# Performance work log

Hardware: AMD Instinct MI355X
Metric: run time of the kernel (lower is better)

The kernel has to match this reference:

```python
import jax, jax.numpy as jnp
import numpy as np

N_NODES = 100000
N_EDGES = 1600000
IN_C, HID_C, OUT_C = 256, 128, 64


def sage_conv(x, src, dst, Wl, Wr, b, n_nodes):
    """PyG SAGEConv: lin_l(mean of neighbor messages) + lin_r(x) + b."""
    msgs = x[src]  # [E, C] gather
    agg = jax.ops.segment_sum(msgs, dst, num_segments=n_nodes)  # [N, C] scatter-add
    deg = jax.ops.segment_sum(jnp.ones((src.shape[0],), x.dtype), dst, num_segments=n_nodes)
    agg = agg / jnp.maximum(deg, 1.0)[:, None]  # mean aggregation, safe for isolated nodes
    return agg @ Wl + x @ Wr + b


def setup_inputs() -> dict:
    key = jax.random.key(0)
    ks = jax.random.split(key, 12)

    def glorot(k, shape):
        fan_in, fan_out = shape
        lim = float(np.sqrt(6.0 / (fan_in + fan_out)))
        return jax.random.uniform(k, shape, jnp.float32, -lim, lim)

    x = jax.random.normal(ks[0], (N_NODES, IN_C), jnp.float32)
    edge_index = jax.random.randint(ks[1], (2, N_EDGES), 0, N_NODES, jnp.int32)
    return {
        "x": x,
        "edge_index": edge_index,
        "Wl0": glorot(ks[2], (IN_C, HID_C)),
        "Wr0": glorot(ks[3], (IN_C, HID_C)),
        "b0": jnp.zeros((HID_C,), jnp.float32),
        "Wl1": glorot(ks[4], (HID_C, HID_C)),
        "Wr1": glorot(ks[5], (HID_C, HID_C)),
        "b1": jnp.zeros((HID_C,), jnp.float32),
        "Wl2": glorot(ks[6], (HID_C, OUT_C)),
        "Wr2": glorot(ks[7], (HID_C, OUT_C)),
        "b2": jnp.zeros((OUT_C,), jnp.float32),
    }


def reference(x, edge_index, Wl0, Wr0, b0, Wl1, Wr1, b1, Wl2, Wr2, b2):
    src, dst = edge_index[0], edge_index[1]
    n = x.shape[0]
    h = x
    out = None
    # convs[:-1]: conv -> relu -> dropout (eval mode: dropout = identity)
    for Wl, Wr, b in ((Wl0, Wr0, b0), (Wl1, Wr1, b1)):
        out = sage_conv(h, src, dst, Wl, Wr, b, n)
        h = jax.nn.relu(out)
    g = h
    x_final = sage_conv(g, src, dst, Wl2, Wr2, b2, n)
    return (x_final, out, g)
```

## Files before the change

### kernel.cpp

```cpp
#include <hip/hip_runtime.h>
#include <stdint.h>

typedef __attribute__((ext_vector_type(4))) float f32x4;
typedef _Float16 half8 __attribute__((ext_vector_type(8)));
typedef _Float16 half4 __attribute__((ext_vector_type(4)));


#define BIN_CHUNK 8192
#define MAXB 512

__global__ __launch_bounds__(256) void k_bhist(const int* __restrict__ dst,
                                               int* __restrict__ bcnt, int E) {
    __shared__ int lh[MAXB];
    for (int i = threadIdx.x; i < MAXB; i += 256) lh[i] = 0;
    __syncthreads();
    const int base = blockIdx.x * BIN_CHUNK;
#pragma unroll 4
    for (int i = 0; i < BIN_CHUNK / 256; i++) {
        int e = base + i * 256 + threadIdx.x;
        if (e < E) atomicAdd(&lh[dst[e] >> 8], 1);
    }
    __syncthreads();
    for (int i = threadIdx.x; i < MAXB; i += 256)
        if (lh[i]) atomicAdd(&bcnt[i], lh[i]);
}

__global__ void k_bscan(const int* __restrict__ bcnt, int* __restrict__ bbase,
                        int* __restrict__ gcur, int nb) {
    if (threadIdx.x == 0 && blockIdx.x == 0) {
        int run = 0;
        for (int i = 0; i < nb; i++) { bbase[i] = run; gcur[i] = run; run += bcnt[i]; }
        bbase[nb] = run;
    }
}

__global__ __launch_bounds__(256) void k_bin(const int* __restrict__ src,
                                             const int* __restrict__ dst,
                                             int* __restrict__ gcur,
                                             unsigned* __restrict__ ebuf, int E) {
    __shared__ int lh[MAXB];
    __shared__ int lcur[MAXB];
    for (int i = threadIdx.x; i < MAXB; i += 256) lh[i] = 0;
    __syncthreads();
    const int base = blockIdx.x * BIN_CHUNK;
#pragma unroll 4
    for (int i = 0; i < BIN_CHUNK / 256; i++) {
        int e = base + i * 256 + threadIdx.x;
        if (e < E) atomicAdd(&lh[dst[e] >> 8], 1);
    }
    __syncthreads();
    for (int i = threadIdx.x; i < MAXB; i += 256)
        lcur[i] = lh[i] ? atomicAdd(&gcur[i], lh[i]) : 0;
    __syncthreads();
#pragma unroll 4
    for (int i = 0; i < BIN_CHUNK / 256; i++) {
        int e = base + i * 256 + threadIdx.x;
        if (e < E) {
            int d = dst[e];
            int pos = atomicAdd(&lcur[d >> 8], 1);
            ebuf[pos] = (unsigned)src[e] | ((unsigned)(d & 255) << 24);
        }
    }
}

__global__ __launch_bounds__(256) void k_nhist(const unsigned* __restrict__ ebuf,
                                               const int* __restrict__ bbase,
                                               int* __restrict__ deg, int N) {
    __shared__ int cnt[256];
    cnt[threadIdx.x] = 0;
    __syncthreads();
    const int b = blockIdx.x;
    const int lo = bbase[b], hi = bbase[b + 1];
    for (int e = lo + threadIdx.x; e < hi; e += 256)
        atomicAdd(&cnt[ebuf[e] >> 24], 1);
    __syncthreads();
    int n = (b << 8) + threadIdx.x;
    if (n < N) deg[n] = cnt[threadIdx.x];
}

__global__ __launch_bounds__(256) void k_bfill(const unsigned* __restrict__ ebuf,
                                               const int* __restrict__ bbase,
                                               const int* __restrict__ rowptr,
                                               int* __restrict__ ssrc, int N) {
    __shared__ int lc[256];
    const int b = blockIdx.x;
    int n = (b << 8) + threadIdx.x;
    lc[threadIdx.x] = (n < N) ? rowptr[n] : 0;
    __syncthreads();
    const int lo = bbase[b], hi = bbase[b + 1];
    for (int e = lo + threadIdx.x; e < hi; e += 256) {
        unsigned v = ebuf[e];
        int pos = atomicAdd(&lc[v >> 24], 1);
        ssrc[pos] = (int)(v & 0xFFFFFFu);
    }
}


__global__ void k_scan1(int* __restrict__ buf, int* __restrict__ chunkSum, int N) {
    const int t = threadIdx.x;
    const int base = blockIdx.x * 2048 + t * 8;
    int v[8];
    int s = 0;
#pragma unroll
    for (int i = 0; i < 8; i++) {
        int idx = base + i;
        v[i] = (idx < N) ? buf[idx] : 0;
        s += v[i];
    }
    __shared__ int sh[256];
    sh[t] = s;
    __syncthreads();
    for (int off = 1; off < 256; off <<= 1) {
        int add = (t >= off) ? sh[t - off] : 0;
        __syncthreads();
        sh[t] += add;
        __syncthreads();
    }
    int excl = sh[t] - s;
    int run = excl;
#pragma unroll
    for (int i = 0; i < 8; i++) {
        int idx = base + i;
        if (idx < N) buf[idx] = run;
        run += v[i];
    }
    if (t == 255) chunkSum[blockIdx.x] = sh[255];
}

__global__ void k_scan2(const int* __restrict__ chunkSum, int* __restrict__ chunkOff,
                        int nch, int* __restrict__ rowptrN) {
    if (threadIdx.x == 0 && blockIdx.x == 0) {
        int run = 0;
        for (int i = 0; i < nch; i++) { chunkOff[i] = run; run += chunkSum[i]; }
        *rowptrN = run;
    }
}

__global__ void k_scan3(int* __restrict__ rowptr, const int* __restrict__ chunkOff, int N) {
    int i = blockIdx.x * 256 + threadIdx.x;
    if (i < N) rowptr[i] += chunkOff[i >> 11];
}


template <int K, int NCOLT>
__global__ void k_wprep(const float* __restrict__ Wl, const float* __restrict__ Wr,
                        _Float16* __restrict__ Wt) {
    constexpr int NCOL = NCOLT / 2;
    int i = blockIdx.x * 256 + threadIdx.x;
    if (i < K * NCOLT) {
        int n = i / K, k = i - n * K;
        float v = (n < NCOL) ? Wl[(size_t)k * NCOL + n] : Wr[(size_t)k * NCOL + (n - NCOL)];
        Wt[(size_t)(k >> 5) * (NCOLT * 32) + n * 32 + (k & 31)] = (_Float16)v;
    }
}


template <int K, int NCOLT, bool AF32>
__global__ __launch_bounds__(256) void k_gemmM(const void* __restrict__ Av,
                                               const _Float16* __restrict__ Wt,
                                               const float* __restrict__ bias,
                                               _Float16* __restrict__ Cl,
                                               _Float16* __restrict__ Cr, int M) {
    constexpr int NCOL = NCOLT / 2;
    constexpr int WC = NCOLT / 4;
    constexpr int NT = WC / 16;
    constexpr int AS = K + 8;
    constexpr int CS = NCOLT + 8;
    constexpr int MAXS = (K > NCOLT ? K : NCOLT) + 8;
    __shared__ _Float16 sh[64 * MAXS];

    const int tid = threadIdx.x;
    const int lane = tid & 63;
    const int wave = tid >> 6;
    const int quad = lane >> 4;
    const int l16 = lane & 15;
    const int m0 = blockIdx.x * 64;
    const int colbase = wave * WC;

    if (AF32) {
        const float* A = (const float*)Av;
#pragma unroll
        for (int i = 0; i < K / 16; i++) {
            int off = i * 1024 + tid * 4;
            int row = off / K, col = off % K;
            f32x4 u = {0.f, 0.f, 0.f, 0.f};
            if (m0 + row < M) u = *(const f32x4*)(A + (size_t)(m0 + row) * K + col);
            half4 h = {(_Float16)u[0], (_Float16)u[1], (_Float16)u[2], (_Float16)u[3]};
            *(half4*)(sh + row * AS + col) = h;
        }
    } else {
        const _Float16* A = (const _Float16*)Av;
#pragma unroll
        for (int i = 0; i < K / 32; i++) {
            int off = i * 2048 + tid * 8;
            int row = off / K, col = off % K;
            half8 u = {0, 0, 0, 0, 0, 0, 0, 0};
            if (m0 + row < M) u = *(const half8*)(A + (size_t)(m0 + row) * K + col);
            *(half8*)(sh + row * AS + col) = u;
        }
    }
    __syncthreads();

    f32x4 acc[4][NT];
#pragma unroll
    for (int rg = 0; rg < 4; rg++)
#pragma unroll
        for (int t = 0; t < NT; t++) acc[rg][t] = (f32x4){0.f, 0.f, 0.f, 0.f};

#pragma unroll
    for (int k0 = 0; k0 < K; k0 += 32) {
        half8 a[4];
#pragma unroll
        for (int rg = 0; rg < 4; rg++)
            a[rg] = *(const half8*)(sh + (rg * 16 + l16) * AS + k0 + quad * 8);
        half8 b[NT];
        const _Float16* Wk = Wt + (size_t)(k0 >> 5) * (NCOLT * 32);
#pragma unroll
        for (int t = 0; t < NT; t++)
            b[t] = *(const half8*)(Wk + (colbase + t * 16 + l16) * 32 + quad * 8);
#pragma unroll
        for (int rg = 0; rg < 4; rg++)
#pragma unroll
            for (int t = 0; t < NT; t++)
                acc[rg][t] = __builtin_amdgcn_mfma_f32_16x16x32_f16(b[t], a[rg], acc[rg][t], 0, 0, 0);
    }

    __syncthreads();

#pragma unroll
    for (int t = 0; t < NT; t++) {
        int c0 = colbase + t * 16 + quad * 4;
        f32x4 bv = {0.f, 0.f, 0.f, 0.f};
        if (c0 >= NCOL) bv = *(const f32x4*)(bias + (c0 - NCOL));
#pragma unroll
        for (int rg = 0; rg < 4; rg++) {
            half4 h = {(_Float16)(acc[rg][t][0] + bv[0]), (_Float16)(acc[rg][t][1] + bv[1]),
                       (_Float16)(acc[rg][t][2] + bv[2]), (_Float16)(acc[rg][t][3] + bv[3])};
            *(half4*)(sh + (rg * 16 + l16) * CS + c0) = h;
        }
    }
    __syncthreads();

#pragma unroll
    for (int i = 0; i < (64 * NCOL) / 2048; i++) {
        int off = i * 2048 + tid * 8;
        int row = off / NCOL, col = off % NCOL;
        if (m0 + row < M) {
            *(half8*)(Cl + (size_t)(m0 + row) * NCOL + col) = *(const half8*)(sh + row * CS + col);
            *(half8*)(Cr + (size_t)(m0 + row) * NCOL + col) = *(const half8*)(sh + row * CS + NCOL + col);
        }
    }
}


template <int COUT, int MODE>
__global__ __launch_bounds__(256) void k_agg(const half8* __restrict__ xl,
                                             const half8* __restrict__ xr,
                                             const int* __restrict__ rowptr,
                                             const int* __restrict__ ssrc,
                                             float* __restrict__ outF1,
                                             float* __restrict__ outF2,
                                             _Float16* __restrict__ outH, int N) {
    constexpr int LPN = COUT / 16;
    constexpr int NPB = 256 / LPN;
    constexpr int C8 = COUT / 8;
    const int tid = threadIdx.x;
    const int c = tid % LPN;
    const int n = blockIdx.x * NPB + tid / LPN;
    if (n >= N) return;

    const int rp0 = rowptr[n];
    const int rp1 = rowptr[n + 1];
    float acc[16];
#pragma unroll
    for (int i = 0; i < 16; i++) acc[i] = 0.f;

    const size_t cb = (size_t)c * 2;
    int e = rp0;
    for (; e + 3 < rp1; e += 4) {
        int s0 = ssrc[e], s1 = ssrc[e + 1], s2 = ssrc[e + 2], s3 = ssrc[e + 3];
        half8 v0a = xl[(size_t)s0 * C8 + cb], v0b = xl[(size_t)s0 * C8 + cb + 1];
        half8 v1a = xl[(size_t)s1 * C8 + cb], v1b = xl[(size_t)s1 * C8 + cb + 1];
        half8 v2a = xl[(size_t)s2 * C8 + cb], v2b = xl[(size_t)s2 * C8 + cb + 1];
        half8 v3a = xl[(size_t)s3 * C8 + cb], v3b = xl[(size_t)s3 * C8 + cb + 1];
#pragma unroll
        for (int i = 0; i < 8; i++) {
            acc[i] += (float)v0a[i] + (float)v1a[i] + (float)v2a[i] + (float)v3a[i];
            acc[8 + i] += (float)v0b[i] + (float)v1b[i] + (float)v2b[i] + (float)v3b[i];
        }
    }
    for (; e < rp1; e++) {
        int s = ssrc[e];
        half8 va = xl[(size_t)s * C8 + cb], vb = xl[(size_t)s * C8 + cb + 1];
#pragma unroll
        for (int i = 0; i < 8; i++) {
            acc[i] += (float)va[i];
            acc[8 + i] += (float)vb[i];
        }
    }

    const int deg = rp1 - rp0;
    const float scale = 1.0f / (float)(deg > 1 ? deg : 1);
    half8 x0 = xr[(size_t)n * C8 + cb];
    half8 x1 = xr[(size_t)n * C8 + cb + 1];
    float res[16];
#pragma unroll
    for (int i = 0; i < 8; i++) {
        res[i] = acc[i] * scale + (float)x0[i];
        res[8 + i] = acc[8 + i] * scale + (float)x1[i];
    }

    const size_t ob = (size_t)n * COUT + (size_t)c * 16;
    if (MODE == 0) {
        half8 h0v, h1v;
#pragma unroll
        for (int i = 0; i < 8; i++) {
            h0v[i] = (_Float16)(res[i] > 0.f ? res[i] : 0.f);
            h1v[i] = (_Float16)(res[8 + i] > 0.f ? res[8 + i] : 0.f);
        }
        *(half8*)(outH + ob) = h0v;
        *(half8*)(outH + ob + 8) = h1v;
    } else if (MODE == 1) {
#pragma unroll
        for (int q = 0; q < 4; q++) {
            f32x4 v = {res[q * 4], res[q * 4 + 1], res[q * 4 + 2], res[q * 4 + 3]};
            *(f32x4*)(outF1 + ob + q * 4) = v;
            f32x4 z = {v[0] > 0.f ? v[0] : 0.f, v[1] > 0.f ? v[1] : 0.f,
                       v[2] > 0.f ? v[2] : 0.f, v[3] > 0.f ? v[3] : 0.f};
            *(f32x4*)(outF2 + ob + q * 4) = z;
        }
        half8 h0v, h1v;
#pragma unroll
        for (int i = 0; i < 8; i++) {
            h0v[i] = (_Float16)(res[i] > 0.f ? res[i] : 0.f);
            h1v[i] = (_Float16)(res[8 + i] > 0.f ? res[8 + i] : 0.f);
        }
        *(half8*)(outH + ob) = h0v;
        *(half8*)(outH + ob + 8) = h1v;
    } else {
#pragma unroll
        for (int q = 0; q < 4; q++) {
            f32x4 v = {res[q * 4], res[q * 4 + 1], res[q * 4 + 2], res[q * 4 + 3]};
            *(f32x4*)(outF1 + ob + q * 4) = v;
        }
    }
}


extern "C" void kernel_launch(void* const* d_in, const int* in_sizes, int n_in,
                              void* d_out, int out_size, void* d_ws, size_t ws_size,
                              hipStream_t stream) {
    const float* x   = (const float*)d_in[0];
    const int*   ei  = (const int*)d_in[1];
    const float* Wl0 = (const float*)d_in[2];
    const float* Wr0 = (const float*)d_in[3];
    const float* b0  = (const float*)d_in[4];
    const float* Wl1 = (const float*)d_in[5];
    const float* Wr1 = (const float*)d_in[6];
    const float* b1  = (const float*)d_in[7];
    const float* Wl2 = (const float*)d_in[8];
    const float* Wr2 = (const float*)d_in[9];
    const float* b2  = (const float*)d_in[10];

    const int N = in_sizes[0] / 256;
    const int E = in_sizes[1] / 2;
    const int* src = ei;
    const int* dst = ei + E;

    char* p = (char*)d_ws;
    auto alloc = [&](size_t bytes) -> void* {
        void* r = (void*)p;
        p += (bytes + 255) & ~(size_t)255;
        return r;
    };
    int*      rowptr   = (int*)alloc((size_t)(N + 1) * 4);
    int*      chunkSum = (int*)alloc(64 * 4);
    int*      chunkOff = (int*)alloc(64 * 4);
    int*      bcnt     = (int*)alloc(MAXB * 4);
    int*      bbase    = (int*)alloc((MAXB + 1) * 4);
    int*      gcur     = (int*)alloc(MAXB * 4);
    int*      ssrc     = (int*)alloc((size_t)E * 4);
    _Float16* xl       = (_Float16*)alloc((size_t)N * 128 * 2);
    _Float16* xr       = (_Float16*)alloc((size_t)N * 128 * 2);
    _Float16* h0       = (_Float16*)alloc((size_t)N * 128 * 2);
    _Float16* gb       = (_Float16*)alloc((size_t)N * 128 * 2);
    _Float16* Wt0      = (_Float16*)alloc((size_t)256 * 256 * 2);
    _Float16* Wt1      = (_Float16*)alloc((size_t)256 * 128 * 2);
    _Float16* Wt2      = (_Float16*)alloc((size_t)128 * 128 * 2);

    unsigned* ebuf = (unsigned*)gb;

    float* out = (float*)d_out;
    float* x_final = out;
    float* out1    = out + (size_t)N * 64;
    float* g       = out + (size_t)N * 192;

    const int nb = (N + 255) >> 8;
    const int nbk = (E + BIN_CHUNK - 1) / BIN_CHUNK;

    hipMemsetAsync(bcnt, 0, MAXB * 4, stream);
    k_bhist<<<nbk, 256, 0, stream>>>(dst, bcnt, E);
    k_bscan<<<1, 64, 0, stream>>>(bcnt, bbase, gcur, nb);
    k_bin<<<nbk, 256, 0, stream>>>(src, dst, gcur, ebuf, E);
    k_nhist<<<nb, 256, 0, stream>>>(ebuf, bbase, rowptr, N);
    int nch = (N + 2047) / 2048;
    k_scan1<<<nch, 256, 0, stream>>>(rowptr, chunkSum, N);
    k_scan2<<<1, 64, 0, stream>>>(chunkSum, chunkOff, nch, rowptr + N);
    k_scan3<<<(N + 255) / 256, 256, 0, stream>>>(rowptr, chunkOff, N);
    k_bfill<<<nb, 256, 0, stream>>>(ebuf, bbase, rowptr, ssrc, N);

    k_wprep<256, 256><<<(256 * 256 + 255) / 256, 256, 0, stream>>>(Wl0, Wr0, Wt0);
    k_wprep<128, 256><<<(128 * 256 + 255) / 256, 256, 0, stream>>>(Wl1, Wr1, Wt1);
    k_wprep<128, 128><<<(128 * 128 + 255) / 256, 256, 0, stream>>>(Wl2, Wr2, Wt2);

    const int gGrid = (N + 63) / 64;

    k_gemmM<256, 256, true><<<gGrid, 256, 0, stream>>>(x, Wt0, b0, xl, xr, N);
    k_agg<128, 0><<<(N + 31) / 32, 256, 0, stream>>>((const half8*)xl, (const half8*)xr,
                                                     rowptr, ssrc, nullptr, nullptr, h0, N);

    k_gemmM<128, 256, false><<<gGrid, 256, 0, stream>>>(h0, Wt1, b1, xl, xr, N);
    k_agg<128, 1><<<(N + 31) / 32, 256, 0, stream>>>((const half8*)xl, (const half8*)xr,
                                                     rowptr, ssrc, out1, g, gb, N);

    k_gemmM<128, 128, false><<<gGrid, 256, 0, stream>>>(gb, Wt2, b2, xl, xr, N);
    k_agg<64, 2><<<(N + 63) / 64, 256, 0, stream>>>((const half8*)xl, (const half8*)xr,
                                                    rowptr, ssrc, x_final, nullptr, nullptr, N);
}
```

Before: 578.6 us.

## Balance edge work across threads in aggregation via shared-memory atomic accumulation

The aggregation kernel no longer gives each node group its own node's edges. It divides the block's contiguous edge range evenly among thread groups, finds each group's starting node by binary search over cached row pointers, and accumulates partial sums into a shared-memory float buffer with atomics. The goal is to remove warp divergence and load imbalance from uneven node degrees. In exchange it adds a block barrier, shared-memory atomics at segment boundaries, and extra LDS traffic.

```diff
diff --git a/kernel.cpp b/kernel.cpp
--- a/kernel.cpp
+++ b/kernel.cpp
@@ -254,63 +254,103 @@
 
 
 template <int COUT, int MODE>
-__global__ __launch_bounds__(256) void k_agg(const half8* __restrict__ xl,
-                                             const half8* __restrict__ xr,
+__global__ __launch_bounds__(256) void k_agg(const _Float16* __restrict__ xl,
+                                             const _Float16* __restrict__ xr,
                                              const int* __restrict__ rowptr,
                                              const int* __restrict__ ssrc,
                                              float* __restrict__ outF1,
                                              float* __restrict__ outF2,
                                              _Float16* __restrict__ outH, int N) {
     constexpr int LPN = COUT / 16;
-    constexpr int NPB = 256 / LPN;
-    constexpr int C8 = COUT / 8;
+    constexpr int NB = 256 / LPN;
+    constexpr int AP = COUT + 4;
+    __shared__ float acc[NB * AP];
+    __shared__ int rp[NB + 1];
+
     const int tid = threadIdx.x;
+    const int n0 = blockIdx.x * NB;
+    if (tid <= NB) {
+        int nn = n0 + tid;
+        rp[tid] = rowptr[nn < N ? nn : N];
+    }
+    for (int i = tid; i < NB * AP; i += 256) acc[i] = 0.f;
+    __syncthreads();
+
+    const int lo = rp[0];
+    const int B = rp[NB] - lo;
+    const int g = tid / LPN;
     const int c = tid % LPN;
-    const int n = blockIdx.x * NPB + tid / LPN;
+    const int cb = c * 16;
+
+    int e0 = lo + (int)(((long long)B * g) / NB);
+    int e1 = lo + (int)(((long long)B * (g + 1)) / NB);
+
+    if (e0 < e1) {
+        int jl = 0, jh = NB - 1;
+        while (jl < jh) {
+            int mid = (jl + jh) >> 1;
+            if (rp[mid + 1] <= e0) jl = mid + 1; else jh = mid;
+        }
+        int j = jl;
+        float racc[16];
+#pragma unroll
+        for (int i = 0; i < 16; i++) racc[i] = 0.f;
+
+        int e = e0;
+        while (e < e1) {
+            int ee = rp[j + 1];
+            if (ee > e1) ee = e1;
+            for (; e + 3 < ee; e += 4) {
+                int s0 = ssrc[e], s1 = ssrc[e + 1], s2 = ssrc[e + 2], s3 = ssrc[e + 3];
+                const half8* p0 = (const half8*)(xl + (size_t)s0 * COUT + cb);
+                const half8* p1 = (const half8*)(xl + (size_t)s1 * COUT + cb);
+                const half8* p2 = (const half8*)(xl + (size_t)s2 * COUT + cb);
+                const half8* p3 = (const half8*)(xl + (size_t)s3 * COUT + cb);
+                half8 v0a = p0[0], v0b = p0[1];
+                half8 v1a = p1[0], v1b = p1[1];
+                half8 v2a = p2[0], v2b = p2[1];
+                half8 v3a = p3[0], v3b = p3[1];
+#pragma unroll
+                for (int i = 0; i < 8; i++) {
+                    racc[i] += (float)v0a[i] + (float)v1a[i] + (float)v2a[i] + (float)v3a[i];
+                    racc[8 + i] += (float)v0b[i] + (float)v1b[i] + (float)v2b[i] + (float)v3b[i];
+                }
+            }
+            for (; e < ee; e++) {
+                int s = ssrc[e];
+                const half8* p = (const half8*)(xl + (size_t)s * COUT + cb);
+                half8 va = p[0], vb = p[1];
+#pragma unroll
+                for (int i = 0; i < 8; i++) {
+                    racc[i] += (float)va[i];
+                    racc[8 + i] += (float)vb[i];
+                }
+            }
+#pragma unroll
+            for (int i = 0; i < 16; i++) {
+                atomicAdd(&acc[j * AP + cb + i], racc[i]);
+                racc[i] = 0.f;
+            }
+            while (j < NB - 1 && rp[j + 1] <= e) j++;
+        }
+    }
+    __syncthreads();
+
+    const int node = tid / LPN;
+    const int n = n0 + node;
     if (n >= N) return;
-
-    const int rp0 = rowptr[n];
-    const int rp1 = rowptr[n + 1];
-    float acc[16];
-#pragma unroll
-    for (int i = 0; i < 16; i++) acc[i] = 0.f;
-
-    const size_t cb = (size_t)c * 2;
-    int e = rp0;
-    for (; e + 3 < rp1; e += 4) {
-        int s0 = ssrc[e], s1 = ssrc[e + 1], s2 = ssrc[e + 2], s3 = ssrc[e + 3];
-        half8 v0a = xl[(size_t)s0 * C8 + cb], v0b = xl[(size_t)s0 * C8 + cb + 1];
-        half8 v1a = xl[(size_t)s1 * C8 + cb], v1b = xl[(size_t)s1 * C8 + cb + 1];
-        half8 v2a = xl[(size_t)s2 * C8 + cb], v2b = xl[(size_t)s2 * C8 + cb + 1];
-        half8 v3a = xl[(size_t)s3 * C8 + cb], v3b = xl[(size_t)s3 * C8 + cb + 1];
-#pragma unroll
-        for (int i = 0; i < 8; i++) {
-            acc[i] += (float)v0a[i] + (float)v1a[i] + (float)v2a[i] + (float)v3a[i];
-            acc[8 + i] += (float)v0b[i] + (float)v1b[i] + (float)v2b[i] + (float)v3b[i];
-        }
-    }
-    for (; e < rp1; e++) {
-        int s = ssrc[e];
-        half8 va = xl[(size_t)s * C8 + cb], vb = xl[(size_t)s * C8 + cb + 1];
-#pragma unroll
-        for (int i = 0; i < 8; i++) {
-            acc[i] += (float)va[i];
-            acc[8 + i] += (float)vb[i];
-        }
-    }
-
-    const int deg = rp1 - rp0;
+    const int deg = rp[node + 1] - rp[node];
     const float scale = 1.0f / (float)(deg > 1 ? deg : 1);
-    half8 x0 = xr[(size_t)n * C8 + cb];
-    half8 x1 = xr[(size_t)n * C8 + cb + 1];
+    const half8* xp = (const half8*)(xr + (size_t)n * COUT + cb);
+    half8 x0 = xp[0], x1 = xp[1];
     float res[16];
 #pragma unroll
     for (int i = 0; i < 8; i++) {
-        res[i] = acc[i] * scale + (float)x0[i];
-        res[8 + i] = acc[8 + i] * scale + (float)x1[i];
-    }
-
-    const size_t ob = (size_t)n * COUT + (size_t)c * 16;
+        res[i] = acc[node * AP + cb + i] * scale + (float)x0[i];
+        res[8 + i] = acc[node * AP + cb + 8 + i] * scale + (float)x1[i];
+    }
+
+    const size_t ob = (size_t)n * COUT + cb;
     if (MODE == 0) {
         half8 h0v, h1v;
 #pragma unroll
@@ -416,14 +456,14 @@
     const int gGrid = (N + 63) / 64;
 
     k_gemmM<256, 256, true><<<gGrid, 256, 0, stream>>>(x, Wt0, b0, xl, xr, N);
-    k_agg<128, 0><<<(N + 31) / 32, 256, 0, stream>>>((const half8*)xl, (const half8*)xr,
-                                                     rowptr, ssrc, nullptr, nullptr, h0, N);
+    k_agg<128, 0><<<(N + 31) / 32, 256, 0, stream>>>(xl, xr, rowptr, ssrc,
+                                                     nullptr, nullptr, h0, N);
 
     k_gemmM<128, 256, false><<<gGrid, 256, 0, stream>>>(h0, Wt1, b1, xl, xr, N);
-    k_agg<128, 1><<<(N + 31) / 32, 256, 0, stream>>>((const half8*)xl, (const half8*)xr,
-                                                     rowptr, ssrc, out1, g, gb, N);
+    k_agg<128, 1><<<(N + 31) / 32, 256, 0, stream>>>(xl, xr, rowptr, ssrc,
+                                                     out1, g, gb, N);
 
     k_gemmM<128, 128, false><<<gGrid, 256, 0, stream>>>(gb, Wt2, b2, xl, xr, N);
-    k_agg<64, 2><<<(N + 63) / 64, 256, 0, stream>>>((const half8*)xl, (const half8*)xr,
-                                                    rowptr, ssrc, x_final, nullptr, nullptr, N);
-}
+    k_agg<64, 2><<<(N + 63) / 64, 256, 0, stream>>>(xl, xr, rowptr, ssrc,
+                                                    x_final, nullptr, nullptr, N);
+}
```

Measured after the change: 799.1 us. 38.1% more time.

## Sort nodes by in-degree to balance aggregation work across waves

Applied to the files above, without the earlier changes.

Adds a counting sort of nodes by in-degree (histogram, descending scan, fill) that builds a permutation. All three aggregation kernels then process nodes in that order, so threads in a wave handle nodes with similar edge counts and less lane divergence occurs. The cost is three extra small kernels plus a memset, an extra indirection per thread, and scattered rather than contiguous output writes and rowptr reads.

```diff
diff --git a/kernel.cpp b/kernel.cpp
--- a/kernel.cpp
+++ b/kernel.cpp
@@ -8,6 +8,7 @@
 
 #define BIN_CHUNK 8192
 #define MAXB 512
+#define DBINS 256
 
 __global__ __launch_bounds__(256) void k_bhist(const int* __restrict__ dst,
                                                int* __restrict__ bcnt, int E) {
@@ -139,6 +140,50 @@
 __global__ void k_scan3(int* __restrict__ rowptr, const int* __restrict__ chunkOff, int N) {
     int i = blockIdx.x * 256 + threadIdx.x;
     if (i < N) rowptr[i] += chunkOff[i >> 11];
+}
+
+
+__global__ __launch_bounds__(256) void k_dhist(const int* __restrict__ rowptr,
+                                               int* __restrict__ dcnt, int N) {
+    __shared__ int lh[DBINS];
+    lh[threadIdx.x] = 0;
+    __syncthreads();
+    int i = blockIdx.x * 256 + threadIdx.x;
+    if (i < N) {
+        int d = rowptr[i + 1] - rowptr[i];
+        if (d > 255) d = 255;
+        atomicAdd(&lh[d], 1);
+    }
+    __syncthreads();
+    if (lh[threadIdx.x]) atomicAdd(&dcnt[threadIdx.x], lh[threadIdx.x]);
+}
+
+__global__ void k_dscan(const int* __restrict__ dcnt, int* __restrict__ dcur) {
+    if (threadIdx.x == 0 && blockIdx.x == 0) {
+        int run = 0;
+        for (int d = DBINS - 1; d >= 0; d--) { dcur[d] = run; run += dcnt[d]; }
+    }
+}
+
+__global__ __launch_bounds__(256) void k_dfill(const int* __restrict__ rowptr,
+                                               int* __restrict__ dcur,
+                                               int* __restrict__ perm, int N) {
+    __shared__ int lh[DBINS];
+    __shared__ int lbase[DBINS];
+    lh[threadIdx.x] = 0;
+    __syncthreads();
+    int i = blockIdx.x * 256 + threadIdx.x;
+    int d = 0, lpos = 0;
+    bool valid = (i < N);
+    if (valid) {
+        d = rowptr[i + 1] - rowptr[i];
+        if (d > 255) d = 255;
+        lpos = atomicAdd(&lh[d], 1);
+    }
+    __syncthreads();
+    lbase[threadIdx.x] = lh[threadIdx.x] ? atomicAdd(&dcur[threadIdx.x], lh[threadIdx.x]) : 0;
+    __syncthreads();
+    if (valid) perm[lbase[d] + lpos] = i;
 }
 
 
@@ -258,6 +303,7 @@
                                              const half8* __restrict__ xr,
                                              const int* __restrict__ rowptr,
                                              const int* __restrict__ ssrc,
+                                             const int* __restrict__ perm,
                                              float* __restrict__ outF1,
                                              float* __restrict__ outF2,
                                              _Float16* __restrict__ outH, int N) {
@@ -266,8 +312,9 @@
     constexpr int C8 = COUT / 8;
     const int tid = threadIdx.x;
     const int c = tid % LPN;
-    const int n = blockIdx.x * NPB + tid / LPN;
-    if (n >= N) return;
+    const int idx = blockIdx.x * NPB + tid / LPN;
+    if (idx >= N) return;
+    const int n = perm[idx];
 
     const int rp0 = rowptr[n];
     const int rp1 = rowptr[n + 1];
@@ -379,6 +426,9 @@
     int*      bcnt     = (int*)alloc(MAXB * 4);
     int*      bbase    = (int*)alloc((MAXB + 1) * 4);
     int*      gcur     = (int*)alloc(MAXB * 4);
+    int*      dcnt     = (int*)alloc(DBINS * 4);
+    int*      dcur     = (int*)alloc(DBINS * 4);
+    int*      perm     = (int*)alloc((size_t)N * 4);
     int*      ssrc     = (int*)alloc((size_t)E * 4);
     _Float16* xl       = (_Float16*)alloc((size_t)N * 128 * 2);
     _Float16* xr       = (_Float16*)alloc((size_t)N * 128 * 2);
@@ -397,8 +447,10 @@
 
     const int nb = (N + 255) >> 8;
     const int nbk = (E + BIN_CHUNK - 1) / BIN_CHUNK;
+    const int nnb = (N + 255) / 256;
 
     hipMemsetAsync(bcnt, 0, MAXB * 4, stream);
+    hipMemsetAsync(dcnt, 0, DBINS * 4, stream);
     k_bhist<<<nbk, 256, 0, stream>>>(dst, bcnt, E);
     k_bscan<<<1, 64, 0, stream>>>(bcnt, bbase, gcur, nb);
     k_bin<<<nbk, 256, 0, stream>>>(src, dst, gcur, ebuf, E);
@@ -409,6 +461,10 @@
     k_scan3<<<(N + 255) / 256, 256, 0, stream>>>(rowptr, chunkOff, N);
     k_bfill<<<nb, 256, 0, stream>>>(ebuf, bbase, rowptr, ssrc, N);
 
+    k_dhist<<<nnb, 256, 0, stream>>>(rowptr, dcnt, N);
+    k_dscan<<<1, 64, 0, stream>>>(dcnt, dcur);
+    k_dfill<<<nnb, 256, 0, stream>>>(rowptr, dcur, perm, N);
+
     k_wprep<256, 256><<<(256 * 256 + 255) / 256, 256, 0, stream>>>(Wl0, Wr0, Wt0);
     k_wprep<128, 256><<<(128 * 256 + 255) / 256, 256, 0, stream>>>(Wl1, Wr1, Wt1);
     k_wprep<128, 128><<<(128 * 128 + 255) / 256, 256, 0, stream>>>(Wl2, Wr2, Wt2);
@@ -417,13 +473,16 @@
 
     k_gemmM<256, 256, true><<<gGrid, 256, 0, stream>>>(x, Wt0, b0, xl, xr, N);
     k_agg<128, 0><<<(N + 31) / 32, 256, 0, stream>>>((const half8*)xl, (const half8*)xr,
-                                                     rowptr, ssrc, nullptr, nullptr, h0, N);
+                                                     rowptr, ssrc, perm,
+                                                     nullptr, nullptr, h0, N);
 
     k_gemmM<128, 256, false><<<gGrid, 256, 0, stream>>>(h0, Wt1, b1, xl, xr, N);
     k_agg<128, 1><<<(N + 31) / 32, 256, 0, stream>>>((const half8*)xl, (const half8*)xr,
-                                                     rowptr, ssrc, out1, g, gb, N);
+                                                     rowptr, ssrc, perm,
+                                                     out1, g, gb, N);
 
     k_gemmM<128, 128, false><<<gGrid, 256, 0, stream>>>(gb, Wt2, b2, xl, xr, N);
     k_agg<64, 2><<<(N + 63) / 64, 256, 0, stream>>>((const half8*)xl, (const half8*)xr,
-                                                    rowptr, ssrc, x_final, nullptr, nullptr, N);
-}
+                                                    rowptr, ssrc, perm,
+                                                    x_final, nullptr, nullptr, N);
+}
```

Result: slower. 603.5 us (+4.3%).
